# Optimization experiments

Hardware: AMD Instinct MI355X
Metric: run time of the kernel (lower is better)

Reference implementation:

```python
import jax, jax.numpy as jnp
import numpy as np

B, N, D, L = 8, 128, 512, 48
NUM_GCN_LAYERS = 2


def setup_inputs() -> dict:
    key = jax.random.key(0)
    ks = jax.random.split(key, 10)
    gcn_inputs = jax.random.normal(ks[0], (B, N, D), dtype=jnp.float32)
    word_seq_len = jax.random.randint(ks[1], (B,), 1, N + 1)
    adj_matrix = jax.random.randint(ks[2], (B, N, N), 0, 2).astype(jnp.float32)
    dep_label_matrix = jax.random.randint(ks[3], (B, N, N), 0, L)
    # per-label weight matrices, stored (L, out_dim, in_dim) as consumed by the bmm
    w_params = jax.random.normal(ks[4], (L, D, D), dtype=jnp.float32) * 0.05
    mlp_w0 = jax.random.normal(ks[5], (D, D), dtype=jnp.float32) * (1.0 / np.sqrt(D))
    mlp_b0 = jnp.zeros((D,), dtype=jnp.float32)
    mlp_w1 = jax.random.normal(ks[6], (D, D), dtype=jnp.float32) * (1.0 / np.sqrt(D))
    mlp_b1 = jnp.zeros((D,), dtype=jnp.float32)
    return {
        'gcn_inputs': gcn_inputs,
        'word_seq_len': word_seq_len,
        'adj_matrix': adj_matrix,
        'dep_label_matrix': dep_label_matrix,
        'w_params': w_params,
        'mlp_w0': mlp_w0,
        'mlp_b0': mlp_b0,
        'mlp_w1': mlp_w1,
        'mlp_b1': mlp_b1,
    }


def reference(gcn_inputs, word_seq_len, adj_matrix, dep_label_matrix,
              w_params, mlp_w0, mlp_b0, mlp_w1, mlp_b1):
    # denom: in-degree + 1 (self)
    denom = adj_matrix.sum(axis=2, keepdims=True) + 1.0  # (B, N, 1)
    b_idx = jnp.arange(B)[:, None, None]                  # (B,1,1)
    j_idx = jnp.arange(N)[None, None, :]                  # (1,1,N)
    h = gcn_inputs
    for _ in range(NUM_GCN_LAYERS):
        # transform every node by every label matrix: (B, L, N, D)
        t = jnp.einsum('ldk,bjk->bljd', w_params, h)
        # gather per-edge label transform: g[b,i,j,:] = t[b, lab[b,i,j], j, :]
        g = t[b_idx, dep_label_matrix, j_idx]             # (B, N, N, D)
        msg = (adj_matrix[..., None] * g).sum(axis=2)     # (B, N, D)
        h = jax.nn.relu(msg / denom)
    x = jax.nn.relu(h @ mlp_w0.T + mlp_b0)
    x = jax.nn.relu(x @ mlp_w1.T + mlp_b1)
    return x
```

## Files before the change

### kernel.cpp

```cpp
#include <hip/hip_runtime.h>
#include <hip/hip_bf16.h>


typedef unsigned short u16;
typedef unsigned int u32;
using bf16x8 = __bf16 __attribute__((ext_vector_type(8)));
using f32x4 = float __attribute__((ext_vector_type(4)));

__device__ __forceinline__ u16 f2bf(float f) {
  u32 u = __float_as_uint(f);
  u32 r = u + 0x7fffu + ((u >> 16) & 1u);
  return (u16)(r >> 16);
}
__device__ __forceinline__ float bf2f(u16 h) {
  return __uint_as_float(((u32)h) << 16);
}

__global__ __launch_bounds__(256)
void cvt_f32_bf16(const float* __restrict__ in, u16* __restrict__ out, int n4) {
  int stride = gridDim.x * blockDim.x;
  for (int i = blockIdx.x * blockDim.x + threadIdx.x; i < n4; i += stride) {
    float4 v = ((const float4*)in)[i];
    uint2 o;
    o.x = (u32)f2bf(v.x) | ((u32)f2bf(v.y) << 16);
    o.y = (u32)f2bf(v.z) | ((u32)f2bf(v.w) << 16);
    ((uint2*)out)[i] = o;
  }
}

#define BM 128
#define BN 128
#define BK 32

__device__ __forceinline__ void gl_lds16(const u16* g, u16* l) {
  __builtin_amdgcn_global_load_lds(
      (const __attribute__((address_space(1))) u32*)g,
      (__attribute__((address_space(3))) u32*)l, 16, 0, 0);
}

__global__ __launch_bounds__(256)
void gemm_nt_bf16(const u16* __restrict__ A, const u16* __restrict__ B,
                  u16* __restrict__ C, int M, int N, int K) {
  __shared__ u16 sA[2][BM * BK];
  __shared__ u16 sB[2][BN * BK];
  const int tid = threadIdx.x;
  const int lane = tid & 63;
  const int wid = tid >> 6;
  const int wm = wid >> 1;
  const int wn = wid & 1;
  const int m0 = blockIdx.y * BM;
  const int n0 = blockIdx.x * BN;

  const int srow = tid >> 2;
  const int scol = (tid & 3) * 8;
  const u16* gA0 = A + (size_t)(m0 + srow) * K + scol;
  const u16* gA1 = A + (size_t)(m0 + 64 + srow) * K + scol;
  const u16* gB0 = B + (size_t)(n0 + srow) * K + scol;
  const u16* gB1 = B + (size_t)(n0 + 64 + srow) * K + scol;

  auto stage = [&](int buf, int kt) {
    const int ko = kt * BK;
    gl_lds16(gA0 + ko, &sA[buf][tid * 8]);
    gl_lds16(gA1 + ko, &sA[buf][2048 + tid * 8]);
    gl_lds16(gB0 + ko, &sB[buf][tid * 8]);
    gl_lds16(gB1 + ko, &sB[buf][2048 + tid * 8]);
  };

  f32x4 acc[4][4];
#pragma unroll
  for (int i = 0; i < 4; ++i)
#pragma unroll
    for (int j = 0; j < 4; ++j)
      acc[i][j] = (f32x4){0.f, 0.f, 0.f, 0.f};

  const int NT = K / BK;
  stage(0, 0);
  asm volatile("s_waitcnt vmcnt(0)" ::: "memory");
  __syncthreads();

  const int r15 = lane & 15;
  const int ksub = (lane >> 4) * 8;
  int cur = 0;
  for (int kt = 0; kt < NT; ++kt) {
    if (kt + 1 < NT) stage(cur ^ 1, kt + 1);

    bf16x8 af[4], bfr[4];
#pragma unroll
    for (int mi = 0; mi < 4; ++mi)
      af[mi] = *(const bf16x8*)&sA[cur][(wm * 64 + mi * 16 + r15) * BK + ksub];
#pragma unroll
    for (int ni = 0; ni < 4; ++ni)
      bfr[ni] = *(const bf16x8*)&sB[cur][(wn * 64 + ni * 16 + r15) * BK + ksub];

#pragma unroll
    for (int mi = 0; mi < 4; ++mi)
#pragma unroll
      for (int ni = 0; ni < 4; ++ni)
        acc[mi][ni] = __builtin_amdgcn_mfma_f32_16x16x32_bf16(
            af[mi], bfr[ni], acc[mi][ni], 0, 0, 0);

    asm volatile("s_waitcnt vmcnt(0)" ::: "memory");
    __syncthreads();
    cur ^= 1;
  }

  const int rq = (lane >> 4) * 4;
#pragma unroll
  for (int mi = 0; mi < 4; ++mi) {
#pragma unroll
    for (int ni = 0; ni < 4; ++ni) {
      const int row = m0 + wm * 64 + mi * 16 + rq;
      const int col = n0 + wn * 64 + ni * 16 + r15;
      const size_t base = (size_t)row * N + col;
      f32x4 v = acc[mi][ni];
#pragma unroll
      for (int r = 0; r < 4; ++r)
        C[base + (size_t)r * N] = f2bf(v[r]);
    }
  }
}

__global__ __launch_bounds__(256)
void gcn_agg(const u16* __restrict__ T, const float* __restrict__ adj,
             const int* __restrict__ lab, u16* __restrict__ Hout) {
  const int bi = blockIdx.x;
  const int b = bi >> 7;
  const int tid = threadIdx.x;
  __shared__ float s_adj[128];
  __shared__ int s_off[128];
  if (tid < 128) {
    s_adj[tid] = adj[(size_t)bi * 128 + tid];
    const int lv = lab[(size_t)bi * 128 + tid];
    s_off[tid] = ((b * 128 + tid) * 48 + lv) * 512;
  }
  __syncthreads();

  const int d = tid * 2;
  float den = 1.0f, a0 = 0.f, a1 = 0.f;
#pragma unroll 8
  for (int j = 0; j < 128; ++j) {
    const float a = s_adj[j];
    den += a;
    const u32 u = *(const u32*)&T[(size_t)s_off[j] + d];
    a0 = fmaf(a, __uint_as_float((u & 0xffffu) << 16), a0);
    a1 = fmaf(a, __uint_as_float(u & 0xffff0000u), a1);
  }
  const float r = 1.0f / den;
  a0 = fmaxf(a0 * r, 0.0f);
  a1 = fmaxf(a1 * r, 0.0f);
  const u32 o = (u32)f2bf(a0) | ((u32)f2bf(a1) << 16);
  *(u32*)&Hout[(size_t)bi * 512 + d] = o;
}

template <bool A_BF16>
__global__ __launch_bounds__(256)
void mlp_gemm(const void* __restrict__ Ain, const float* __restrict__ W,
              const float* __restrict__ bias, float* __restrict__ out,
              int M, int N, int K) {
  const int tid = threadIdx.x;
  const int tx = tid & 15;
  const int ty = tid >> 4;
  const int n0 = blockIdx.x * 64;
  const int m0 = blockIdx.y * 64;
  __shared__ float sA[64][17];
  __shared__ float sB[64][17];
  float acc[4][4] = {};

  for (int k0 = 0; k0 < K; k0 += 16) {
#pragma unroll
    for (int i = 0; i < 4; ++i) {
      const int idx = tid + i * 256;
      const int rr = idx >> 4;
      const int cc = idx & 15;
      float av;
      if (A_BF16)
        av = bf2f(((const u16*)Ain)[(size_t)(m0 + rr) * K + k0 + cc]);
      else
        av = ((const float*)Ain)[(size_t)(m0 + rr) * K + k0 + cc];
      sA[rr][cc] = av;
      sB[rr][cc] = W[(size_t)(n0 + rr) * K + k0 + cc];
    }
    __syncthreads();
#pragma unroll
    for (int k = 0; k < 16; ++k) {
      float ar[4], bc[4];
#pragma unroll
      for (int r = 0; r < 4; ++r) ar[r] = sA[ty * 4 + r][k];
#pragma unroll
      for (int c = 0; c < 4; ++c) bc[c] = sB[tx * 4 + c][k];
#pragma unroll
      for (int r = 0; r < 4; ++r)
#pragma unroll
        for (int c = 0; c < 4; ++c)
          acc[r][c] = fmaf(ar[r], bc[c], acc[r][c]);
    }
    __syncthreads();
  }
#pragma unroll
  for (int r = 0; r < 4; ++r) {
#pragma unroll
    for (int c = 0; c < 4; ++c) {
      const int row = m0 + ty * 4 + r;
      const int col = n0 + tx * 4 + c;
      out[(size_t)row * N + col] = fmaxf(acc[r][c] + bias[col], 0.0f);
    }
  }
}

extern "C" void kernel_launch(void* const* d_in, const int* in_sizes, int n_in,
                              void* d_out, int out_size, void* d_ws, size_t ws_size,
                              hipStream_t stream) {
  const float* gcn_inputs = (const float*)d_in[0];
  const float* adj = (const float*)d_in[2];
  const int* lab = (const int*)d_in[3];
  const float* w_params = (const float*)d_in[4];
  const float* w0 = (const float*)d_in[5];
  const float* b0 = (const float*)d_in[6];
  const float* w1 = (const float*)d_in[7];
  const float* b1 = (const float*)d_in[8];
  float* out = (float*)d_out;

  char* ws = (char*)d_ws;
  u16* Wbf = (u16*)ws;
  u16* T = (u16*)(ws + 25165824);
  u16* Ha = (u16*)(ws + 75497472);
  u16* Hb = (u16*)(ws + 76546048);
  float* X1 = (float*)(ws + 77594624);

  cvt_f32_bf16<<<2048, 256, 0, stream>>>(w_params, Wbf, (48 * 512 * 512) / 4);
  cvt_f32_bf16<<<512, 256, 0, stream>>>(gcn_inputs, Ha, (8 * 128 * 512) / 4);

  dim3 gg(24576 / BN, 1024 / BM);

  gemm_nt_bf16<<<gg, 256, 0, stream>>>(Ha, Wbf, T, 1024, 24576, 512);
  gcn_agg<<<1024, 256, 0, stream>>>(T, adj, lab, Hb);
  gemm_nt_bf16<<<gg, 256, 0, stream>>>(Hb, Wbf, T, 1024, 24576, 512);
  gcn_agg<<<1024, 256, 0, stream>>>(T, adj, lab, Ha);

  dim3 gm(512 / 64, 1024 / 64);
  mlp_gemm<true><<<gm, 256, 0, stream>>>(Ha, w0, b0, X1, 1024, 512, 512);
  mlp_gemm<false><<<gm, 256, 0, stream>>>(X1, w1, b1, out, 1024, 512, 512);
}
```

Baseline: 210.4 us.

## Run output MLP on bf16 MFMA GEMM with hi/lo split-precision operands

Replaces the scalar fp32 tiled MLP GEMMs with the existing bf16 MFMA GEMM kernel. To keep near-fp32 accuracy it splits weights and activations into bf16 hi and lo parts and concatenates them along K (1024 and 1536). The first GEMM's fused epilogue adds bias, applies ReLU and writes the split operand for the second GEMM. This costs a weight-prep kernel and 2-3x more MMA work per MLP layer, but moves that work off the slow FP32 FMA path onto matrix cores.

```diff
diff --git a/kernel.cpp b/kernel.cpp
--- a/kernel.cpp
+++ b/kernel.cpp
@@ -28,6 +28,29 @@
   }
 }
 
+__global__ __launch_bounds__(256)
+void prep_mlp_w(const float* __restrict__ w0, const float* __restrict__ w1,
+                u16* __restrict__ Bp1, u16* __restrict__ Bp2) {
+  int idx = blockIdx.x * 256 + threadIdx.x;
+  if (idx < 262144) {
+    const int n = idx >> 9, k = idx & 511;
+    const float v = w0[idx];
+    const u16 hi = f2bf(v);
+    const float lo = v - bf2f(hi);
+    Bp1[n * 1024 + k] = hi;
+    Bp1[n * 1024 + 512 + k] = f2bf(lo);
+  } else {
+    const int j = idx - 262144;
+    const int n = j >> 9, k = j & 511;
+    const float v = w1[j];
+    const u16 hi = f2bf(v);
+    const float lo = v - bf2f(hi);
+    Bp2[n * 1536 + k] = hi;
+    Bp2[n * 1536 + 512 + k] = f2bf(lo);
+    Bp2[n * 1536 + 1024 + k] = hi;
+  }
+}
+
 #define BM 128
 #define BN 128
 #define BK 32
@@ -38,9 +61,11 @@
       (__attribute__((address_space(3))) u32*)l, 16, 0, 0);
 }
 
+template <int EPI>
 __global__ __launch_bounds__(256)
 void gemm_nt_bf16(const u16* __restrict__ A, const u16* __restrict__ B,
-                  u16* __restrict__ C, int M, int N, int K) {
+                  void* __restrict__ C, const float* __restrict__ bias,
+                  int N, int K, int ldc) {
   __shared__ u16 sA[2][BM * BK];
   __shared__ u16 sB[2][BN * BK];
   const int tid = threadIdx.x;
@@ -111,15 +136,38 @@
     for (int ni = 0; ni < 4; ++ni) {
       const int row = m0 + wm * 64 + mi * 16 + rq;
       const int col = n0 + wn * 64 + ni * 16 + r15;
-      const size_t base = (size_t)row * N + col;
       f32x4 v = acc[mi][ni];
-#pragma unroll
-      for (int r = 0; r < 4; ++r)
-        C[base + (size_t)r * N] = f2bf(v[r]);
+      if (EPI == 0) {
+        u16* Cb = (u16*)C;
+        const size_t base = (size_t)row * ldc + col;
+#pragma unroll
+        for (int r = 0; r < 4; ++r)
+          Cb[base + (size_t)r * ldc] = f2bf(v[r]);
+      } else if (EPI == 1) {
+        u16* Cb = (u16*)C;
+        const float bv = bias[col];
+#pragma unroll
+        for (int r = 0; r < 4; ++r) {
+          const float x = fmaxf(v[r] + bv, 0.0f);
+          const u16 hi = f2bf(x);
+          const float lo = x - bf2f(hi);
+          const size_t base = (size_t)(row + r) * 1536 + col;
+          Cb[base] = hi;
+          Cb[base + 512] = hi;
+          Cb[base + 1024] = f2bf(lo);
+        }
+      } else {
+        float* Cf = (float*)C;
+        const float bv = bias[col];
+#pragma unroll
+        for (int r = 0; r < 4; ++r)
+          Cf[(size_t)(row + r) * ldc + col] = fmaxf(v[r] + bv, 0.0f);
+      }
     }
   }
 }
 
+template <bool DUP>
 __global__ __launch_bounds__(256)
 void gcn_agg(const u16* __restrict__ T, const float* __restrict__ adj,
              const int* __restrict__ lab, u16* __restrict__ Hout) {
@@ -149,61 +197,11 @@
   a0 = fmaxf(a0 * r, 0.0f);
   a1 = fmaxf(a1 * r, 0.0f);
   const u32 o = (u32)f2bf(a0) | ((u32)f2bf(a1) << 16);
-  *(u32*)&Hout[(size_t)bi * 512 + d] = o;
-}
-
-template <bool A_BF16>
-__global__ __launch_bounds__(256)
-void mlp_gemm(const void* __restrict__ Ain, const float* __restrict__ W,
-              const float* __restrict__ bias, float* __restrict__ out,
-              int M, int N, int K) {
-  const int tid = threadIdx.x;
-  const int tx = tid & 15;
-  const int ty = tid >> 4;
-  const int n0 = blockIdx.x * 64;
-  const int m0 = blockIdx.y * 64;
-  __shared__ float sA[64][17];
-  __shared__ float sB[64][17];
-  float acc[4][4] = {};
-
-  for (int k0 = 0; k0 < K; k0 += 16) {
-#pragma unroll
-    for (int i = 0; i < 4; ++i) {
-      const int idx = tid + i * 256;
-      const int rr = idx >> 4;
-      const int cc = idx & 15;
-      float av;
-      if (A_BF16)
-        av = bf2f(((const u16*)Ain)[(size_t)(m0 + rr) * K + k0 + cc]);
-      else
-        av = ((const float*)Ain)[(size_t)(m0 + rr) * K + k0 + cc];
-      sA[rr][cc] = av;
-      sB[rr][cc] = W[(size_t)(n0 + rr) * K + k0 + cc];
-    }
-    __syncthreads();
-#pragma unroll
-    for (int k = 0; k < 16; ++k) {
-      float ar[4], bc[4];
-#pragma unroll
-      for (int r = 0; r < 4; ++r) ar[r] = sA[ty * 4 + r][k];
-#pragma unroll
-      for (int c = 0; c < 4; ++c) bc[c] = sB[tx * 4 + c][k];
-#pragma unroll
-      for (int r = 0; r < 4; ++r)
-#pragma unroll
-        for (int c = 0; c < 4; ++c)
-          acc[r][c] = fmaf(ar[r], bc[c], acc[r][c]);
-    }
-    __syncthreads();
-  }
-#pragma unroll
-  for (int r = 0; r < 4; ++r) {
-#pragma unroll
-    for (int c = 0; c < 4; ++c) {
-      const int row = m0 + ty * 4 + r;
-      const int col = n0 + tx * 4 + c;
-      out[(size_t)row * N + col] = fmaxf(acc[r][c] + bias[col], 0.0f);
-    }
+  if (DUP) {
+    *(u32*)&Hout[(size_t)bi * 1024 + d] = o;
+    *(u32*)&Hout[(size_t)bi * 1024 + 512 + d] = o;
+  } else {
+    *(u32*)&Hout[(size_t)bi * 512 + d] = o;
   }
 }
 
@@ -223,21 +221,26 @@
   char* ws = (char*)d_ws;
   u16* Wbf = (u16*)ws;
   u16* T = (u16*)(ws + 25165824);
+  u16* Bp1 = T;
+  u16* Bp2 = (u16*)(ws + 25165824 + (1 << 20));
   u16* Ha = (u16*)(ws + 75497472);
   u16* Hb = (u16*)(ws + 76546048);
-  float* X1 = (float*)(ws + 77594624);
+  u16* Ap1 = (u16*)(ws + 77594624);
+  u16* Ap2 = (u16*)(ws + 79691776);
 
   cvt_f32_bf16<<<2048, 256, 0, stream>>>(w_params, Wbf, (48 * 512 * 512) / 4);
   cvt_f32_bf16<<<512, 256, 0, stream>>>(gcn_inputs, Ha, (8 * 128 * 512) / 4);
 
   dim3 gg(24576 / BN, 1024 / BM);
 
-  gemm_nt_bf16<<<gg, 256, 0, stream>>>(Ha, Wbf, T, 1024, 24576, 512);
-  gcn_agg<<<1024, 256, 0, stream>>>(T, adj, lab, Hb);
-  gemm_nt_bf16<<<gg, 256, 0, stream>>>(Hb, Wbf, T, 1024, 24576, 512);
-  gcn_agg<<<1024, 256, 0, stream>>>(T, adj, lab, Ha);
-
-  dim3 gm(512 / 64, 1024 / 64);
-  mlp_gemm<true><<<gm, 256, 0, stream>>>(Ha, w0, b0, X1, 1024, 512, 512);
-  mlp_gemm<false><<<gm, 256, 0, stream>>>(X1, w1, b1, out, 1024, 512, 512);
-}
+  gemm_nt_bf16<0><<<gg, 256, 0, stream>>>(Ha, Wbf, T, nullptr, 24576, 512, 24576);
+  gcn_agg<false><<<1024, 256, 0, stream>>>(T, adj, lab, Hb);
+  gemm_nt_bf16<0><<<gg, 256, 0, stream>>>(Hb, Wbf, T, nullptr, 24576, 512, 24576);
+  gcn_agg<true><<<1024, 256, 0, stream>>>(T, adj, lab, Ap1);
+
+  prep_mlp_w<<<2048, 256, 0, stream>>>(w0, w1, Bp1, Bp2);
+
+  dim3 gm(512 / BN, 1024 / BM);
+  gemm_nt_bf16<1><<<gm, 256, 0, stream>>>(Ap1, Bp1, Ap2, b0, 512, 1024, 1536);
+  gemm_nt_bf16<2><<<gm, 256, 0, stream>>>(Ap2, Bp2, out, b1, 512, 1536, 512);
+}
```

Result: faster. 185.2 us (-12.0%).
